# Performance work log

Measured on AMD Instinct MI355X. Metric: run time of the kernel, lower is better.

Reference implementation:

```python
import jax, jax.numpy as jnp
import numpy as np

DIM = 2048
N_HEADS = 32
N_KV_HEADS = 8
HEAD_DIM = DIM // N_HEADS  # 64
N_REP = N_HEADS // N_KV_HEADS
ROPE_BASE = 10000.0


def rope_tables(seq_len, dim):
    inv_freq = 1.0 / (ROPE_BASE ** (jnp.arange(0, dim, 2, dtype=jnp.float32) / dim))
    t = jnp.arange(seq_len, dtype=jnp.float32)
    freqs = jnp.outer(t, inv_freq)            # [S, dim/2]
    emb = jnp.concatenate([freqs, freqs], -1)  # [S, dim]
    return jnp.cos(emb), jnp.sin(emb)          # each [S, dim]


def rotate_half(x):
    x1, x2 = jnp.split(x, 2, axis=-1)
    return jnp.concatenate([-x2, x1], axis=-1)


def setup_inputs() -> dict:
    key = jax.random.key(0)
    k_x, k_q, k_k, k_v, k_o = jax.random.split(key, 5)
    B, S = 2, 2048
    scale = 0.02
    x = jax.random.normal(k_x, (B, S, DIM), dtype=jnp.float32)
    # torch Linear weights are [out, in]
    w_q = jax.random.normal(k_q, (N_HEADS * HEAD_DIM, DIM), dtype=jnp.float32) * scale
    w_k = jax.random.normal(k_k, (N_KV_HEADS * HEAD_DIM, DIM), dtype=jnp.float32) * scale
    w_v = jax.random.normal(k_v, (N_KV_HEADS * HEAD_DIM, DIM), dtype=jnp.float32) * scale
    w_o = jax.random.normal(k_o, (DIM, N_HEADS * HEAD_DIM), dtype=jnp.float32) * scale
    return {"x": x, "w_q": w_q, "w_k": w_k, "w_v": w_v, "w_o": w_o}


def reference(x, w_q, w_k, w_v, w_o):
    B, S, _ = x.shape
    # projections (torch Linear: x @ W^T), reshape to [B, H, S, D]
    q = jnp.einsum('bsd,ed->bse', x, w_q).reshape(B, S, N_HEADS, HEAD_DIM).transpose(0, 2, 1, 3)
    k = jnp.einsum('bsd,ed->bse', x, w_k).reshape(B, S, N_KV_HEADS, HEAD_DIM).transpose(0, 2, 1, 3)
    v = jnp.einsum('bsd,ed->bse', x, w_v).reshape(B, S, N_KV_HEADS, HEAD_DIM).transpose(0, 2, 1, 3)
    # RoPE
    cos, sin = rope_tables(S, HEAD_DIM)  # [S, D]
    cos = cos[None, None]
    sin = sin[None, None]
    q = q * cos + rotate_half(q) * sin
    k = k * cos + rotate_half(k) * sin
    # GQA: expand kv heads (repeat_interleave along head dim)
    k = jnp.repeat(k, N_REP, axis=1)
    v = jnp.repeat(v, N_REP, axis=1)
    # attention
    scores = jnp.einsum('bhqd,bhkd->bhqk', q, k) / jnp.sqrt(jnp.float32(HEAD_DIM))
    attn = jax.nn.softmax(scores, axis=-1)
    out = jnp.einsum('bhqk,bhkd->bhqd', attn, v)
    out = out.transpose(0, 2, 1, 3).reshape(B, S, N_HEADS * HEAD_DIM)
    return jnp.einsum('bse,de->bsd', out, w_o)
```

## Files before the change

### kernel.cpp

```cpp
#include <hip/hip_runtime.h>
#include <hip/hip_bf16.h>

typedef __attribute__((ext_vector_type(8))) short bf16x8;
typedef __attribute__((ext_vector_type(4))) short bf16x4s;
typedef __attribute__((ext_vector_type(4))) float f32x4;
typedef __attribute__((ext_vector_type(2))) unsigned int u32x2;
typedef unsigned int u32;

#define DIM 2048
#define NH 32
#define NKV 8
#define HD 64
#define BB 2
#define SS 2048
#define MROWS (BB*SS)
#define NQKV 3072
#define KDIM 2048
#define L2E 1.44269504f

__device__ __forceinline__ short f2bf(float f){
  u32 u = __float_as_uint(f);
  u32 r = u + 0x7fffu + ((u >> 16) & 1u);
  return (short)(r >> 16);
}
__device__ __forceinline__ float bf2f(short s){
  return __uint_as_float(((u32)(unsigned short)s) << 16);
}

__device__ __forceinline__ void gload16(const void* g, void* l){
  __builtin_amdgcn_global_load_lds((const __attribute__((address_space(1))) u32*)g,
                                   (__attribute__((address_space(3))) u32*)l, 16, 0, 0);
}

__global__ __launch_bounds__(256) void cvt_all_kernel(const float* __restrict__ x,
                                                      const float* __restrict__ wq,
                                                      const float* __restrict__ wk,
                                                      const float* __restrict__ wv,
                                                      const float* __restrict__ wo,
                                                      short* __restrict__ xb,
                                                      short* __restrict__ wqkvb,
                                                      short* __restrict__ wob,
                                                      float* __restrict__ cosT,
                                                      float* __restrict__ sinT){
  int bid = blockIdx.x;
  if (bid >= 18432){
    int idx = (bid-18432)*256 + threadIdx.x;
    int s = idx >> 5, i = idx & 31;
    float inv = powf(10000.f, -(float)i * (1.f/32.f));
    float f = (float)s * inv;
    cosT[idx] = cosf(f);
    sinT[idx] = sinf(f);
    return;
  }
  int i = bid*256 + threadIdx.x;
  const float* src; short* dst; int off;
  if      (bid <  8192){ src = x;  dst = xb;              off = 0; }
  else if (bid < 12288){ src = wq; dst = wqkvb;           off = 2097152; }
  else if (bid < 13312){ src = wk; dst = wqkvb+2048*2048; off = 3145728; }
  else if (bid < 14336){ src = wv; dst = wqkvb+2560*2048; off = 3407872; }
  else                 { src = wo; dst = wob;             off = 3670016; }
  int j = i - off;
  f32x4 v = ((const f32x4*)src)[j];
  bf16x4s o;
  #pragma unroll
  for (int t=0;t<4;++t) o[t] = f2bf(v[t]);
  ((bf16x4s*)dst)[j] = o;
}

__global__ __launch_bounds__(256) void vT_kernel(const short* __restrict__ qkv,
                                                 short* __restrict__ Vtg){
  __shared__ short T[64*72];
  const int tid = threadIdx.x;
  const int s0 = blockIdx.x*64, hkv = blockIdx.y, b = blockIdx.z;
  const short* vbase = qkv + (size_t)b*SS*NQKV + DIM + NKV*HD + hkv*HD;
  #pragma unroll
  for (int cc=0; cc<2; ++cc){
    int c = tid + cc*256;
    int s = c >> 3, dc = c & 7;
    bf16x8 v = *(const bf16x8*)(vbase + (size_t)(s0+s)*NQKV + dc*8);
    #pragma unroll
    for (int i=0;i<8;++i) T[(dc*8+i)*72 + s] = v[i];
  }
  __syncthreads();
  short* obase = Vtg + ((size_t)(b*NKV + hkv)*64)*SS;
  #pragma unroll
  for (int cc=0; cc<2; ++cc){
    int c = tid + cc*256;
    int d = c >> 3, sc = c & 7;
    *(bf16x8*)(obase + (size_t)d*SS + s0 + sc*8) = *(const bf16x8*)&T[d*72 + sc*8];
  }
}

__global__ __launch_bounds__(256) void gemm_bt_kernel(const short* __restrict__ A,
                                                      const short* __restrict__ Bm,
                                                      short* __restrict__ C,
                                                      int ldc, int K,
                                                      const float* __restrict__ cosT,
                                                      const float* __restrict__ sinT,
                                                      int rope){
  __shared__ short As[128*32];
  __shared__ short Bs[128*32];
  const int tid = threadIdx.x;
  const int wave = tid >> 6, lane = tid & 63;
  const int g = lane >> 4, r16 = lane & 15;
  const int m0 = blockIdx.y * 128, n0 = blockIdx.x * 128;
  const int wr = wave >> 1, wc = wave & 1;
  f32x4 acc[4][4] = {};
  for (int k0 = 0; k0 < K; k0 += 32){
    #pragma unroll
    for (int c2 = 0; c2 < 2; ++c2){
      int ch = (wave*2 + c2)*64 + lane;
      int row = ch >> 2, kc = ch & 3;
      gload16(A  + (size_t)(m0+row)*K + k0 + kc*8, (char*)As + (wave*2+c2)*1024);
      gload16(Bm + (size_t)(n0+row)*K + k0 + kc*8, (char*)Bs + (wave*2+c2)*1024);
    }
    __syncthreads();
    bf16x8 a[4], b[4];
    #pragma unroll
    for (int i=0;i<4;++i)
      a[i] = *(const bf16x8*)&As[(wr*64 + i*16 + r16)*32 + g*8];
    #pragma unroll
    for (int j=0;j<4;++j)
      b[j] = *(const bf16x8*)&Bs[(wc*64 + j*16 + r16)*32 + g*8];
    #pragma unroll
    for (int i=0;i<4;++i)
      #pragma unroll
      for (int j=0;j<4;++j)
        acc[i][j] = __builtin_amdgcn_mfma_f32_16x16x32_bf16(a[i], b[j], acc[i][j], 0, 0, 0);
    __syncthreads();
  }
  if (rope && n0 < 2560){
    float qsc = (n0 < 2048) ? 0.125f : 1.0f;
    #pragma unroll
    for (int i=0;i<4;++i)
      #pragma unroll
      for (int r=0;r<4;++r){
        int row = m0 + wr*64 + i*16 + g*4 + r;
        int s = row & (SS-1);
        #pragma unroll
        for (int j=0;j<2;++j){
          int col = n0 + wc*64 + j*16 + r16;
          float c  = cosT[(s<<5) + (col&31)];
          float sn = sinT[(s<<5) + (col&31)];
          float x1 = acc[i][j][r], x2 = acc[i][j+2][r];
          C[(size_t)row*ldc + col]      = f2bf((x1*c - x2*sn)*qsc);
          C[(size_t)row*ldc + col + 32] = f2bf((x2*c + x1*sn)*qsc);
        }
      }
  } else {
    #pragma unroll
    for (int i=0;i<4;++i)
      #pragma unroll
      for (int j=0;j<4;++j)
        #pragma unroll
        for (int r=0;r<4;++r){
          int row = m0 + wr*64 + i*16 + g*4 + r;
          int col = n0 + wc*64 + j*16 + r16;
          C[(size_t)row*ldc + col] = f2bf(acc[i][j][r]);
        }
  }
}

__global__ __launch_bounds__(256) void gemm_btf_kernel(const short* __restrict__ A,
                                                       const short* __restrict__ Bm,
                                                       float* __restrict__ C,
                                                       int ldc, int K){
  __shared__ short As[128*32];
  __shared__ short Bs[128*32];
  const int tid = threadIdx.x;
  const int wave = tid >> 6, lane = tid & 63;
  const int g = lane >> 4, r16 = lane & 15;
  const int m0 = blockIdx.y * 128, n0 = blockIdx.x * 128;
  const int wr = wave >> 1, wc = wave & 1;
  f32x4 acc[4][4] = {};
  for (int k0 = 0; k0 < K; k0 += 32){
    #pragma unroll
    for (int c2 = 0; c2 < 2; ++c2){
      int ch = (wave*2 + c2)*64 + lane;
      int row = ch >> 2, kc = ch & 3;
      gload16(A  + (size_t)(m0+row)*K + k0 + kc*8, (char*)As + (wave*2+c2)*1024);
      gload16(Bm + (size_t)(n0+row)*K + k0 + kc*8, (char*)Bs + (wave*2+c2)*1024);
    }
    __syncthreads();
    bf16x8 a[4], b[4];
    #pragma unroll
    for (int i=0;i<4;++i)
      a[i] = *(const bf16x8*)&As[(wr*64 + i*16 + r16)*32 + g*8];
    #pragma unroll
    for (int j=0;j<4;++j)
      b[j] = *(const bf16x8*)&Bs[(wc*64 + j*16 + r16)*32 + g*8];
    #pragma unroll
    for (int i=0;i<4;++i)
      #pragma unroll
      for (int j=0;j<4;++j)
        acc[i][j] = __builtin_amdgcn_mfma_f32_16x16x32_bf16(a[i], b[j], acc[i][j], 0, 0, 0);
    __syncthreads();
  }
  #pragma unroll
  for (int i=0;i<4;++i)
    #pragma unroll
    for (int j=0;j<4;++j)
      #pragma unroll
      for (int r=0;r<4;++r){
        int row = m0 + wr*64 + i*16 + g*4 + r;
        int col = n0 + wc*64 + j*16 + r16;
        C[(size_t)row*ldc + col] = acc[i][j][r];
      }
}

__global__ __launch_bounds__(512) void attn_kernel(const short* __restrict__ qkv,
                                                   const short* __restrict__ Vtg,
                                                   short* __restrict__ outb){
  __shared__ short Ks[64*64];
  __shared__ short Vt[64*64];
  __shared__ short Ps[8*16*72];
  const int tid = threadIdx.x;
  const int wave = tid >> 6, lane = tid & 63;
  const int g = lane >> 4, r16 = lane & 15;
  const int qt = blockIdx.x, h = blockIdx.y, b = blockIdx.z;
  const int hkv = h >> 2;
  const size_t row0 = (size_t)b * SS;
  const int qrow0 = qt*128 + wave*16;
  const short* qbase  = qkv + (row0 + qrow0)*NQKV + h*HD;
  const short* kbase  = qkv + row0*NQKV + DIM + hkv*HD;
  const short* vtbase = Vtg + ((size_t)(b*NKV + hkv)*64)*SS;

  bf16x8 qf[2];
  #pragma unroll
  for (int kk=0;kk<2;++kk)
    qf[kk] = *(const bf16x8*)(qbase + (size_t)r16*NQKV + kk*32 + g*8);

  f32x4 oaccT[4] = {};
  float M = -6.0e29f;
  float lrow = 0.f;

  short* pwv = &Ps[wave*16*72];

  const int trow = tid >> 3, tc3 = tid & 7;
  const size_t koff = (size_t)trow*NQKV + ((tc3 ^ (trow&7)) << 3);
  const size_t voff = (size_t)trow*SS   + ((tc3 ^ (trow&7)) << 3);

  auto LOADR = [&](int s0, bf16x8& kr, bf16x8& vr){
    kr = *(const bf16x8*)(kbase + (size_t)s0*NQKV + koff);
    vr = *(const bf16x8*)(vtbase + voff + s0);
  };
  auto WRITE = [&](bf16x8 kr, bf16x8 vr){
    *(bf16x8*)((char*)Ks + tid*16) = kr;
    *(bf16x8*)((char*)Vt + tid*16) = vr;
  };

  { bf16x8 k0r, v0r; LOADR(0, k0r, v0r); WRITE(k0r, v0r); }
  __syncthreads();

  const int NT = SS/64;
  for (int t = 0; t < NT; ++t){
    bool more = (t+1 < NT);
    bf16x8 krn, vrn;
    if (more) LOADR((t+1)*64, krn, vrn);

    f32x4 sacc[4];
    __builtin_amdgcn_s_setprio(1);
    #pragma unroll
    for (int t2=0;t2<4;++t2){
      f32x4 cacc = {};
      #pragma unroll
      for (int kk=0;kk<2;++kk){
        int krow = t2*16 + r16;
        const bf16x8* kp = (const bf16x8*)((const char*)Ks + krow*128 +
                            ((((kk<<2)+g) ^ (krow&7)) << 4));
        cacc = __builtin_amdgcn_mfma_f32_16x16x32_bf16(*kp, qf[kk], cacc, 0,0,0);
      }
      sacc[t2] = cacc;
    }
    __builtin_amdgcn_s_setprio(0);

    float m01 = fmaxf(fmaxf(sacc[0][0], sacc[0][1]), fmaxf(sacc[0][2], sacc[0][3]));
    float m23 = fmaxf(fmaxf(sacc[1][0], sacc[1][1]), fmaxf(sacc[1][2], sacc[1][3]));
    float m45 = fmaxf(fmaxf(sacc[2][0], sacc[2][1]), fmaxf(sacc[2][2], sacc[2][3]));
    float m67 = fmaxf(fmaxf(sacc[3][0], sacc[3][1]), fmaxf(sacc[3][2], sacc[3][3]));
    float mx = fmaxf(fmaxf(m01, m23), fmaxf(m45, m67));
    mx = fmaxf(mx, __shfl_xor(mx, 16));
    mx = fmaxf(mx, __shfl_xor(mx, 32));
    float mxl = mx * L2E;
    if (__any(mxl > M + 11.5f)){
      float Mnew = fmaxf(M, mxl);
      float al;
      { float a = M - Mnew; asm("v_exp_f32 %0, %1" : "=v"(al) : "v"(a)); }
      lrow *= al;
      #pragma unroll
      for (int j=0;j<4;++j)
        #pragma unroll
        for (int r=0;r<4;++r) oaccT[j][r] *= al;
      M = Mnew;
    }
    float s4[4] = {0.f,0.f,0.f,0.f};
    u32 pb[4][2];
    #pragma unroll
    for (int t2=0;t2<4;++t2){
      float p[4];
      #pragma unroll
      for (int r=0;r<4;++r){
        float a = fmaf(sacc[t2][r], L2E, -M);
        asm("v_exp_f32 %0, %1" : "=v"(p[r]) : "v"(a));
        s4[r] += p[r];
      }
      asm("v_cvt_pk_bf16_f32 %0, %1, %2" : "=v"(pb[t2][0]) : "v"(p[0]), "v"(p[1]));
      asm("v_cvt_pk_bf16_f32 %0, %1, %2" : "=v"(pb[t2][1]) : "v"(p[2]), "v"(p[3]));
    }
    float sum = (s4[0]+s4[1]) + (s4[2]+s4[3]);
    sum += __shfl_xor(sum, 16);
    sum += __shfl_xor(sum, 32);
    lrow += sum;

    #pragma unroll
    for (int t2=0;t2<4;++t2)
      *(u32x2*)&pwv[r16*72 + t2*16 + g*4] = (u32x2){pb[t2][0], pb[t2][1]};
    __builtin_amdgcn_s_setprio(1);
    #pragma unroll
    for (int kki=0;kki<2;++kki){
      bf16x8 pf = *(const bf16x8*)&pwv[r16*72 + 32*kki + g*8];
      #pragma unroll
      for (int j=0;j<4;++j){
        int d = j*16 + r16;
        const bf16x8* vp = (const bf16x8*)((const char*)Vt + d*128 +
                            ((((kki<<2)+g) ^ (d&7)) << 4));
        oaccT[j] = __builtin_amdgcn_mfma_f32_16x16x32_bf16(*vp, pf, oaccT[j], 0,0,0);
      }
    }
    __builtin_amdgcn_s_setprio(0);

    if (more){
      __syncthreads();
      WRITE(krn, vrn);
      __syncthreads();
    }
  }

  float inv = 1.0f / lrow;
  short* orow = outb + (row0 + qrow0 + r16)*(size_t)DIM + h*HD;
  #pragma unroll
  for (int j=0;j<4;++j){
    bf16x4s ov;
    #pragma unroll
    for (int r=0;r<4;++r) ov[r] = f2bf(oaccT[j][r]*inv);
    *(bf16x4s*)&orow[j*16 + g*4] = ov;
  }
}

extern "C" void kernel_launch(void* const* d_in, const int* in_sizes, int n_in,
                              void* d_out, int out_size, void* d_ws, size_t ws_size,
                              hipStream_t stream){
  const float* x  = (const float*)d_in[0];
  const float* wq = (const float*)d_in[1];
  const float* wk = (const float*)d_in[2];
  const float* wv = (const float*)d_in[3];
  const float* wo = (const float*)d_in[4];
  float* outf = (float*)d_out;

  char* ws = (char*)d_ws;
  short* wqkvb = (short*)(ws);
  short* attnb = (short*)(ws);
  short* wob   = (short*)(ws + 16777216);
  short* qkv   = (short*)(ws + 25165824);
  float* cosT  = (float*)(ws + 50331648);
  float* sinT  = (float*)(ws + 50593792);
  short* xb    = (short*)d_out;
  short* Vtg   = (short*)((char*)d_out + 16777216);

  cvt_all_kernel<<<18688, 256, 0, stream>>>(x, wq, wk, wv, wo, xb, wqkvb, wob, cosT, sinT);

  gemm_bt_kernel<<<dim3(NQKV/128, MROWS/128), 256, 0, stream>>>(xb, wqkvb, qkv, NQKV, KDIM,
                                                                cosT, sinT, 1);
  vT_kernel<<<dim3(SS/64, NKV, BB), 256, 0, stream>>>(qkv, Vtg);
  attn_kernel<<<dim3(SS/128, NH, BB), 512, 0, stream>>>(qkv, Vtg, attnb);
  gemm_btf_kernel<<<dim3(DIM/128, MROWS/128), 256, 0, stream>>>(attnb, wob, outf, DIM, KDIM);
}
```

Baseline: 252.7 us.

## Deepen GEMM K-tile with swizzled LDS and double attention query tile per block

Both GEMM kernels now stage 64-wide K slices instead of 32, using an XOR swizzle on LDS chunks to avoid bank conflicts. This halves the number of barrier pairs per GEMM. The attention kernel moves to 1024 threads covering 256 query rows, so each K/V tile loaded into LDS serves twice as many queries. The K and V loads are also split across thread halves. The cost is fewer attention blocks (512 in total), larger workgroups and more LDS per block, which may lower occupancy and scheduling flexibility.

Result: faster. 247.3 us (-2.1%).

```diff
diff --git a/kernel.cpp b/kernel.cpp
--- a/kernel.cpp
+++ b/kernel.cpp
@@ -98,35 +98,43 @@
                                                       const float* __restrict__ cosT,
                                                       const float* __restrict__ sinT,
                                                       int rope){
-  __shared__ short As[128*32];
-  __shared__ short Bs[128*32];
+  __shared__ short As[128*64];
+  __shared__ short Bs[128*64];
   const int tid = threadIdx.x;
   const int wave = tid >> 6, lane = tid & 63;
   const int g = lane >> 4, r16 = lane & 15;
   const int m0 = blockIdx.y * 128, n0 = blockIdx.x * 128;
   const int wr = wave >> 1, wc = wave & 1;
   f32x4 acc[4][4] = {};
-  for (int k0 = 0; k0 < K; k0 += 32){
-    #pragma unroll
-    for (int c2 = 0; c2 < 2; ++c2){
-      int ch = (wave*2 + c2)*64 + lane;
-      int row = ch >> 2, kc = ch & 3;
-      gload16(A  + (size_t)(m0+row)*K + k0 + kc*8, (char*)As + (wave*2+c2)*1024);
-      gload16(Bm + (size_t)(n0+row)*K + k0 + kc*8, (char*)Bs + (wave*2+c2)*1024);
+  for (int k0 = 0; k0 < K; k0 += 64){
+    #pragma unroll
+    for (int it = 0; it < 4; ++it){
+      int ch = it*256 + wave*64 + lane;
+      int row = ch >> 3, kc = ch & 7;
+      int skc = kc ^ (row & 7);
+      gload16(A  + (size_t)(m0+row)*K + k0 + skc*8, (char*)As + it*4096 + wave*1024);
+      gload16(Bm + (size_t)(n0+row)*K + k0 + skc*8, (char*)Bs + it*4096 + wave*1024);
     }
     __syncthreads();
-    bf16x8 a[4], b[4];
-    #pragma unroll
-    for (int i=0;i<4;++i)
-      a[i] = *(const bf16x8*)&As[(wr*64 + i*16 + r16)*32 + g*8];
-    #pragma unroll
-    for (int j=0;j<4;++j)
-      b[j] = *(const bf16x8*)&Bs[(wc*64 + j*16 + r16)*32 + g*8];
-    #pragma unroll
-    for (int i=0;i<4;++i)
-      #pragma unroll
-      for (int j=0;j<4;++j)
-        acc[i][j] = __builtin_amdgcn_mfma_f32_16x16x32_bf16(a[i], b[j], acc[i][j], 0, 0, 0);
+    #pragma unroll
+    for (int kk=0; kk<2; ++kk){
+      bf16x8 a[4], b[4];
+      #pragma unroll
+      for (int i=0;i<4;++i){
+        int Ra = wr*64 + i*16 + r16;
+        a[i] = *(const bf16x8*)((const char*)As + Ra*128 + ((((kk<<2)+g) ^ (Ra&7)) << 4));
+      }
+      #pragma unroll
+      for (int j=0;j<4;++j){
+        int Rb = wc*64 + j*16 + r16;
+        b[j] = *(const bf16x8*)((const char*)Bs + Rb*128 + ((((kk<<2)+g) ^ (Rb&7)) << 4));
+      }
+      #pragma unroll
+      for (int i=0;i<4;++i)
+        #pragma unroll
+        for (int j=0;j<4;++j)
+          acc[i][j] = __builtin_amdgcn_mfma_f32_16x16x32_bf16(a[i], b[j], acc[i][j], 0, 0, 0);
+    }
     __syncthreads();
   }
   if (rope && n0 < 2560){
@@ -165,35 +173,43 @@
                                                        const short* __restrict__ Bm,
                                                        float* __restrict__ C,
                                                        int ldc, int K){
-  __shared__ short As[128*32];
-  __shared__ short Bs[128*32];
+  __shared__ short As[128*64];
+  __shared__ short Bs[128*64];
   const int tid = threadIdx.x;
   const int wave = tid >> 6, lane = tid & 63;
   const int g = lane >> 4, r16 = lane & 15;
   const int m0 = blockIdx.y * 128, n0 = blockIdx.x * 128;
   const int wr = wave >> 1, wc = wave & 1;
   f32x4 acc[4][4] = {};
-  for (int k0 = 0; k0 < K; k0 += 32){
-    #pragma unroll
-    for (int c2 = 0; c2 < 2; ++c2){
-      int ch = (wave*2 + c2)*64 + lane;
-      int row = ch >> 2, kc = ch & 3;
-      gload16(A  + (size_t)(m0+row)*K + k0 + kc*8, (char*)As + (wave*2+c2)*1024);
-      gload16(Bm + (size_t)(n0+row)*K + k0 + kc*8, (char*)Bs + (wave*2+c2)*1024);
+  for (int k0 = 0; k0 < K; k0 += 64){
+    #pragma unroll
+    for (int it = 0; it < 4; ++it){
+      int ch = it*256 + wave*64 + lane;
+      int row = ch >> 3, kc = ch & 7;
+      int skc = kc ^ (row & 7);
+      gload16(A  + (size_t)(m0+row)*K + k0 + skc*8, (char*)As + it*4096 + wave*1024);
+      gload16(Bm + (size_t)(n0+row)*K + k0 + skc*8, (char*)Bs + it*4096 + wave*1024);
     }
     __syncthreads();
-    bf16x8 a[4], b[4];
-    #pragma unroll
-    for (int i=0;i<4;++i)
-      a[i] = *(const bf16x8*)&As[(wr*64 + i*16 + r16)*32 + g*8];
-    #pragma unroll
-    for (int j=0;j<4;++j)
-      b[j] = *(const bf16x8*)&Bs[(wc*64 + j*16 + r16)*32 + g*8];
-    #pragma unroll
-    for (int i=0;i<4;++i)
-      #pragma unroll
-      for (int j=0;j<4;++j)
-        acc[i][j] = __builtin_amdgcn_mfma_f32_16x16x32_bf16(a[i], b[j], acc[i][j], 0, 0, 0);
+    #pragma unroll
+    for (int kk=0; kk<2; ++kk){
+      bf16x8 a[4], b[4];
+      #pragma unroll
+      for (int i=0;i<4;++i){
+        int Ra = wr*64 + i*16 + r16;
+        a[i] = *(const bf16x8*)((const char*)As + Ra*128 + ((((kk<<2)+g) ^ (Ra&7)) << 4));
+      }
+      #pragma unroll
+      for (int j=0;j<4;++j){
+        int Rb = wc*64 + j*16 + r16;
+        b[j] = *(const bf16x8*)((const char*)Bs + Rb*128 + ((((kk<<2)+g) ^ (Rb&7)) << 4));
+      }
+      #pragma unroll
+      for (int i=0;i<4;++i)
+        #pragma unroll
+        for (int j=0;j<4;++j)
+          acc[i][j] = __builtin_amdgcn_mfma_f32_16x16x32_bf16(a[i], b[j], acc[i][j], 0, 0, 0);
+    }
     __syncthreads();
   }
   #pragma unroll
@@ -208,19 +224,19 @@
       }
 }
 
-__global__ __launch_bounds__(512) void attn_kernel(const short* __restrict__ qkv,
-                                                   const short* __restrict__ Vtg,
-                                                   short* __restrict__ outb){
+__global__ __launch_bounds__(1024) void attn_kernel(const short* __restrict__ qkv,
+                                                    const short* __restrict__ Vtg,
+                                                    short* __restrict__ outb){
   __shared__ short Ks[64*64];
   __shared__ short Vt[64*64];
-  __shared__ short Ps[8*16*72];
+  __shared__ short Ps[16*16*72];
   const int tid = threadIdx.x;
   const int wave = tid >> 6, lane = tid & 63;
   const int g = lane >> 4, r16 = lane & 15;
   const int qt = blockIdx.x, h = blockIdx.y, b = blockIdx.z;
   const int hkv = h >> 2;
   const size_t row0 = (size_t)b * SS;
-  const int qrow0 = qt*128 + wave*16;
+  const int qrow0 = qt*256 + wave*16;
   const short* qbase  = qkv + (row0 + qrow0)*NQKV + h*HD;
   const short* kbase  = qkv + row0*NQKV + DIM + hkv*HD;
   const short* vtbase = Vtg + ((size_t)(b*NKV + hkv)*64)*SS;
@@ -236,27 +252,27 @@
 
   short* pwv = &Ps[wave*16*72];
 
-  const int trow = tid >> 3, tc3 = tid & 7;
-  const size_t koff = (size_t)trow*NQKV + ((tc3 ^ (trow&7)) << 3);
-  const size_t voff = (size_t)trow*SS   + ((tc3 ^ (trow&7)) << 3);
-
-  auto LOADR = [&](int s0, bf16x8& kr, bf16x8& vr){
-    kr = *(const bf16x8*)(kbase + (size_t)s0*NQKV + koff);
-    vr = *(const bf16x8*)(vtbase + voff + s0);
+  const bool isK = (tid < 512);
+  const int u = isK ? tid : (tid - 512);
+  const int trow = u >> 3, tc3 = u & 7;
+  const size_t goff = isK ? ((size_t)trow*NQKV + ((tc3 ^ (trow&7)) << 3))
+                          : ((size_t)trow*SS   + ((tc3 ^ (trow&7)) << 3));
+  const short* gsrc = isK ? kbase : vtbase;
+  char* ldst = (isK ? (char*)Ks : (char*)Vt) + u*16;
+
+  auto LOADR = [&](int s0, bf16x8& r){
+    r = *(const bf16x8*)(gsrc + goff + (isK ? (size_t)s0*NQKV : (size_t)s0));
   };
-  auto WRITE = [&](bf16x8 kr, bf16x8 vr){
-    *(bf16x8*)((char*)Ks + tid*16) = kr;
-    *(bf16x8*)((char*)Vt + tid*16) = vr;
-  };
-
-  { bf16x8 k0r, v0r; LOADR(0, k0r, v0r); WRITE(k0r, v0r); }
+  auto WRITE = [&](bf16x8 r){ *(bf16x8*)ldst = r; };
+
+  { bf16x8 r0; LOADR(0, r0); WRITE(r0); }
   __syncthreads();
 
   const int NT = SS/64;
   for (int t = 0; t < NT; ++t){
     bool more = (t+1 < NT);
-    bf16x8 krn, vrn;
-    if (more) LOADR((t+1)*64, krn, vrn);
+    bf16x8 rn;
+    if (more) LOADR((t+1)*64, rn);
 
     f32x4 sacc[4];
     __builtin_amdgcn_s_setprio(1);
@@ -331,7 +347,7 @@
 
     if (more){
       __syncthreads();
-      WRITE(krn, vrn);
+      WRITE(rn);
       __syncthreads();
     }
   }
@@ -372,6 +388,6 @@
   gemm_bt_kernel<<<dim3(NQKV/128, MROWS/128), 256, 0, stream>>>(xb, wqkvb, qkv, NQKV, KDIM,
                                                                 cosT, sinT, 1);
   vT_kernel<<<dim3(SS/64, NKV, BB), 256, 0, stream>>>(qkv, Vtg);
-  attn_kernel<<<dim3(SS/128, NH, BB), 512, 0, stream>>>(qkv, Vtg, attnb);
+  attn_kernel<<<dim3(SS/256, NH, BB), 1024, 0, stream>>>(qkv, Vtg, attnb);
   gemm_btf_kernel<<<dim3(DIM/128, MROWS/128), 256, 0, stream>>>(attnb, wob, outf, DIM, KDIM);
 }
```
